# Kernel tuning notes

Hardware: AMD Instinct MI355X
Metric: run time of the kernel (lower is better)

The kernel has to match this reference:

```python
import jax, jax.numpy as jnp
import numpy as np

MASK_VALUE = -10000.0


def setup_inputs() -> dict:
    key = jax.random.key(0)
    ks = jax.random.split(key, 6)
    F_, H, L1N, L2N, B = 1024, 2048, 64, 256, 8192

    def w(k, shape, fan_in):
        return jax.random.normal(k, shape, jnp.float32) * (1.0 / np.sqrt(fan_in))

    x = jax.random.normal(ks[0], (B, F_), jnp.float32)
    W1_1 = w(ks[1], (F_, H), F_); b1_1 = jnp.zeros((H,), jnp.float32)
    W1_2 = w(ks[2], (H, L1N), H); b1_2 = jnp.zeros((L1N,), jnp.float32)
    W2_1 = w(ks[3], (F_, H), F_); b2_1 = jnp.zeros((H,), jnp.float32)
    W2_2 = w(ks[4], (2 * H, L2N), 2 * H); b2_2 = jnp.zeros((L2N,), jnp.float32)
    # child_parent[j] = L1 parent of L2 label j (contiguous groups of 4),
    # equivalent to L12_table = [[4i,4i+1,4i+2,4i+3] for i in range(64)]
    child_parent = jnp.arange(L2N, dtype=jnp.int32) // (L2N // L1N)
    return dict(x=x, W1_1=W1_1, b1_1=b1_1, W1_2=W1_2, b1_2=b1_2,
                W2_1=W2_1, b2_1=b2_1, W2_2=W2_2, b2_2=b2_2,
                child_parent=child_parent)


def reference(x, W1_1, b1_1, W1_2, b1_2, W2_1, b2_1, W2_2, b2_2, child_parent):
    h1 = jax.nn.relu(x @ W1_1 + b1_1)          # [B, H]
    h2 = jax.nn.relu(x @ W2_1 + b2_1)          # [B, H]
    cat = jnp.concatenate([h1, h2], axis=1)    # [B, 2H]
    L1 = jax.nn.softmax(jax.nn.relu(h1 @ W1_2 + b1_2), axis=1)   # [B, L1N]
    l2_logits = jax.nn.relu(cat @ W2_2 + b2_2)                   # [B, L2N]
    parent = jnp.argmax(L1, axis=1)                              # [B] int
    # mask[i, j] = 0 if L2 label j is a child of argmax L1 label, else MASK_VALUE
    mask = jnp.where(child_parent[None, :] == parent[:, None], 0.0, MASK_VALUE)
    L2 = jax.nn.softmax(l2_logits + mask, axis=1)
    return (L1, L2)
```

## Files before the change

### kernel.cpp

```cpp
#include <hip/hip_runtime.h>
#include <hip/hip_bf16.h>
#include <stdint.h>
#include <math.h>


typedef _Float16 f16x8 __attribute__((ext_vector_type(8)));
typedef float    f32x4 __attribute__((ext_vector_type(4)));

#define MASK_VALUE (-10000.0f)
#define SWZ(r) ((((r) + ((r) >> 2))) & 3)
#define SW4(row, c) ((c) ^ (((row) >> 1) & 3))
#define RSCALE 2048.0f
#define INV_RSCALE (1.0f / 2048.0f)

#define GLOBAL_AS __attribute__((address_space(1)))
#define LDS_AS    __attribute__((address_space(3)))

__device__ __forceinline__ void gload16(const void* g, void* lds) {
    __builtin_amdgcn_global_load_lds((const GLOBAL_AS void*)g, (LDS_AS void*)lds, 16, 0, 0);
}

__device__ __forceinline__ float rd_any(const void* p, size_t i, int flag) {
    return flag ? (float)((const __hip_bfloat16*)p)[i] : ((const float*)p)[i];
}

__device__ __forceinline__ void wg_bar() {
    asm volatile("" ::: "memory");
    __builtin_amdgcn_s_barrier();
    asm volatile("" ::: "memory");
}
#define LGKM0() do { asm volatile("s_waitcnt lgkmcnt(0)" ::: "memory"); \
                     __builtin_amdgcn_sched_barrier(0); } while (0)
#define VMW(n)  asm volatile("s_waitcnt vmcnt(" #n ")" ::: "memory")
#define MFMA16(a,b,c) __builtin_amdgcn_mfma_f32_16x16x32_f16((a),(b),(c),0,0,0)

__global__ void detect_dtype(const unsigned int* __restrict__ x, int* __restrict__ flag) {
    __shared__ int cnt;
    if (threadIdx.x == 0) cnt = 0;
    __syncthreads();
    int local = 0;
#pragma unroll
    for (int i = 0; i < 4; ++i) {
        unsigned int w = x[threadIdx.x * 4 + i];
        unsigned int e = (w >> 7) & 0xFFu;
        if (e >= 96u && e <= 144u) local++;
    }
    atomicAdd(&cnt, local);
    __syncthreads();
    if (threadIdx.x == 0) *flag = (cnt >= 600) ? 1 : 0;
}

__global__ void prep_all(
    const void* __restrict__ x, const void* __restrict__ W1_1,
    const void* __restrict__ W2_1, const void* __restrict__ W2_2,
    const void* __restrict__ W1_2,
    _Float16* __restrict__ xh, _Float16* __restrict__ xl,
    _Float16* __restrict__ whT, _Float16* __restrict__ wlT,
    _Float16* __restrict__ W2Tf, _Float16* __restrict__ W22Tf,
    _Float16* __restrict__ w12h, _Float16* __restrict__ w12l,
    const int* __restrict__ flagp)
{
    __shared__ __align__(16) float tile[64][65];
    int flag = *flagp;
    int bid = blockIdx.x, t = threadIdx.x;
    int tx = t & 63, ty = t >> 6;

    if (bid < 8192) {
        size_t i = ((size_t)bid * 256 + t) * 4;
#pragma unroll
        for (int j = 0; j < 4; ++j) {
            float a = rd_any(x, i + j, flag);
            _Float16 h = (_Float16)a;
            xh[i + j] = h;
            xl[i + j] = (_Float16)((a - (float)h) * RSCALE);
        }
        return;
    }

    if (bid < 8704) {
        int b = bid - 8192;
        int c0 = (b & 31) * 64, r0 = (b >> 5) * 64;
#pragma unroll
        for (int i = 0; i < 16; ++i) {
            int r = ty + i * 4;
            tile[r][tx] = rd_any(W1_1, (size_t)(r0 + r) * 2048 + c0 + tx, flag);
        }
        __syncthreads();
#pragma unroll
        for (int i = 0; i < 16; ++i) {
            int r = ty + i * 4;
            size_t o = (size_t)(c0 + r) * 1024 + r0 + tx;
            float a = tile[tx][r];
            _Float16 h = (_Float16)a;
            whT[o] = h;
            wlT[o] = (_Float16)((a - (float)h) * RSCALE);
        }
        return;
    }

    if (bid < 9216) {
        int b = bid - 8704;
        int c0 = (b & 31) * 64, r0 = (b >> 5) * 64;
#pragma unroll
        for (int i = 0; i < 16; ++i) {
            int r = ty + i * 4;
            tile[r][tx] = rd_any(W2_1, (size_t)(r0 + r) * 2048 + c0 + tx, flag);
        }
        __syncthreads();
#pragma unroll
        for (int i = 0; i < 16; ++i) {
            int r = ty + i * 4;
            W2Tf[(size_t)(c0 + r) * 1024 + r0 + tx] = (_Float16)tile[tx][r];
        }
        return;
    }

    if (bid < 9472) {
        int b = bid - 9216;
        int c0 = (b & 3) * 64, r0 = (b >> 2) * 64;
#pragma unroll
        for (int i = 0; i < 16; ++i) {
            int r = ty + i * 4;
            tile[r][tx] = rd_any(W2_2, (size_t)(r0 + r) * 256 + c0 + tx, flag);
        }
        __syncthreads();
#pragma unroll
        for (int i = 0; i < 16; ++i) {
            int r = ty + i * 4;
            W22Tf[(size_t)(c0 + r) * 4096 + r0 + tx] = (_Float16)tile[tx][r];
        }
        return;
    }

    {
        int b = bid - 9472;
        int r0 = b * 64;
#pragma unroll
        for (int i = 0; i < 16; ++i) {
            int r = ty + i * 4;
            tile[r][tx] = rd_any(W1_2, (size_t)(r0 + r) * 64 + tx, flag);
        }
        __syncthreads();
#pragma unroll
        for (int i = 0; i < 16; ++i) {
            int r = ty + i * 4;
            size_t o = (size_t)r * 2048 + r0 + tx;
            float a = tile[tx][r];
            _Float16 h = (_Float16)a;
            w12h[o] = h;
            w12l[o] = (_Float16)((a - (float)h) * RSCALE);
        }
    }
}

__global__ __launch_bounds__(512, 2) void h12_gemm8(
    const _Float16* __restrict__ xh, const _Float16* __restrict__ xl,
    const _Float16* __restrict__ whT, const _Float16* __restrict__ wlT,
    const void* __restrict__ b11,
    const _Float16* __restrict__ W2Tf, const void* __restrict__ b21,
    _Float16* __restrict__ h1h, _Float16* __restrict__ h1l,
    _Float16* __restrict__ h2b,
    const int* __restrict__ flagp)
{
    __shared__ __align__(16) char smem[147456];
    int flag = *flagp;
    int t = threadIdx.x, w = t >> 6, lane = t & 63;
    int ml = lane & 15, q = lane >> 4, rq = q * 4;

    int xcd = blockIdx.x & 7, rblk = blockIdx.x >> 3;

    if (rblk < 64) {
        int lb = xcd * 64 + rblk;
        int mt = lb >> 4, nt = lb & 15;
        int i0 = mt * 256, j0 = nt * 128;
        int wr = w & 3, wc = w >> 2;

        f32x4 acc1[4][4], acc2[4][4];
#pragma unroll
        for (int a = 0; a < 4; ++a)
#pragma unroll
            for (int b = 0; b < 4; ++b) {
                acc1[a][b] = (f32x4){0.f, 0.f, 0.f, 0.f};
                acc2[a][b] = (f32x4){0.f, 0.f, 0.f, 0.f};
            }

        auto stage = [&](char* bp, int kt, int g) {
            if (g < 4) {
                int ci = ((g & 1) << 9) + t;
                int row = ci >> 2;
                int c = SW4(row, ci & 3);
                const _Float16* src = (g < 2) ? xh : xl;
                gload16(src + (size_t)(i0 + row) * 1024 + kt + c * 8,
                        bp + ((g < 2) ? 0 : 16384) + ci * 16);
            } else {
                int ci = t;
                int row = ci >> 2;
                int c = SW4(row, ci & 3);
                const _Float16* src = (g == 4) ? whT : wlT;
                gload16(src + (size_t)(j0 + row) * 1024 + kt + c * 8,
                        bp + ((g == 4) ? 32768 : 40960) + ci * 16);
            }
        };

#pragma unroll
        for (int g = 0; g < 6; ++g) stage(smem, 0, g);
#pragma unroll
        for (int g = 0; g < 6; ++g) stage(smem + 49152, 32, g);
        VMW(6);
        wg_bar();

        int cur = 0;
        for (int s = 0; s < 32; ++s) {
            char* bp = smem + cur * 49152;
            int cur2 = cur + 2; if (cur2 >= 3) cur2 -= 3;
            char* bp2 = smem + cur2 * 49152;
            int kt2 = (s + 2) * 32;
            bool st = (s < 30);

            f16x8 ah[4], al[4], bh[2], bl[2];
            if (st) { stage(bp2, kt2, 0); stage(bp2, kt2, 1); stage(bp2, kt2, 2); }
#pragma unroll
            for (int rt = 0; rt < 4; ++rt) {
                int row = wr * 64 + rt * 16 + ml;
                int off = row * 64 + (SW4(row, q) << 4);
                ah[rt] = *(const f16x8*)(bp + off);
                al[rt] = *(const f16x8*)(bp + 16384 + off);
            }
#pragma unroll
            for (int ct = 0; ct < 2; ++ct) {
                int row = wc * 64 + ct * 16 + ml;
                int off = row * 64 + (SW4(row, q) << 4);
                bh[ct] = *(const f16x8*)(bp + 32768 + off);
                bl[ct] = *(const f16x8*)(bp + 40960 + off);
            }
            LGKM0();
            __builtin_amdgcn_s_setprio(1);
#pragma unroll
            for (int rt = 0; rt < 4; ++rt)
#pragma unroll
                for (int ct = 0; ct < 2; ++ct) {
                    acc1[rt][ct] = MFMA16(ah[rt], bh[ct], acc1[rt][ct]);
                    acc2[rt][ct] = MFMA16(ah[rt], bl[ct], acc2[rt][ct]);
                    acc2[rt][ct] = MFMA16(al[rt], bh[ct], acc2[rt][ct]);
                }
            __builtin_amdgcn_s_setprio(0);

            if (st) { stage(bp2, kt2, 3); stage(bp2, kt2, 4); stage(bp2, kt2, 5); }
#pragma unroll
            for (int ct = 0; ct < 2; ++ct) {
                int row = wc * 64 + (ct + 2) * 16 + ml;
                int off = row * 64 + (SW4(row, q) << 4);
                bh[ct] = *(const f16x8*)(bp + 32768 + off);
                bl[ct] = *(const f16x8*)(bp + 40960 + off);
            }
            LGKM0();
            __builtin_amdgcn_s_setprio(1);
#pragma unroll
            for (int rt = 0; rt < 4; ++rt)
#pragma unroll
                for (int ct = 0; ct < 2; ++ct) {
                    acc1[rt][ct + 2] = MFMA16(ah[rt], bh[ct], acc1[rt][ct + 2]);
                    acc2[rt][ct + 2] = MFMA16(ah[rt], bl[ct], acc2[rt][ct + 2]);
                    acc2[rt][ct + 2] = MFMA16(al[rt], bh[ct], acc2[rt][ct + 2]);
                }
            __builtin_amdgcn_s_setprio(0);

            if (st) { VMW(6); } else { VMW(0); }
            wg_bar();
            cur = cur + 1; if (cur == 3) cur = 0;
        }

#pragma unroll
        for (int ct = 0; ct < 4; ++ct) {
            float bv = rd_any(b11, j0 + wc * 64 + ct * 16 + ml, flag);
#pragma unroll
            for (int rt = 0; rt < 4; ++rt)
#pragma unroll
                for (int rr = 0; rr < 4; ++rr) {
                    float v = acc1[rt][ct][rr] + acc2[rt][ct][rr] * INV_RSCALE + bv;
                    acc1[rt][ct][rr] = v > 0.f ? v : 0.f;
                }
        }
        _Float16* C = (_Float16*)smem;
#pragma unroll
        for (int p = 0; p < 2; ++p) {
            __syncthreads();
#pragma unroll
            for (int rt = 0; rt < 4; ++rt)
#pragma unroll
                for (int ct = 0; ct < 4; ++ct)
#pragma unroll
                    for (int rr = 0; rr < 4; ++rr) {
                        float v = acc1[rt][ct][rr];
                        _Float16 h = (_Float16)v;
                        _Float16 outv = (p == 0) ? h
                                      : (_Float16)((v - (float)h) * RSCALE);
                        int rl = wr * 64 + rt * 16 + rq + rr;
                        int cl = wc * 64 + ct * 16 + ml;
                        C[rl * 136 + cl] = outv;
                    }
            __syncthreads();
            _Float16* dst = (p == 0) ? h1h : h1l;
#pragma unroll
            for (int i = 0; i < 8; ++i) {
                int c = i * 512 + t;
                int row = c >> 4, c8 = (c & 15) * 8;
                *(f16x8*)(dst + (size_t)(i0 + row) * 2048 + j0 + c8) =
                    *(const f16x8*)(C + row * 136 + c8);
            }
        }
    } else {
        int lb = xcd * 32 + (rblk - 64);
        int mt = lb >> 3, nt = lb & 7;
        int i0 = mt * 256, j0 = nt * 256;
        int wr = w & 1, wc = w >> 1;

        f32x4 acc[8][4];
#pragma unroll
        for (int a = 0; a < 8; ++a)
#pragma unroll
            for (int b = 0; b < 4; ++b) acc[a][b] = (f32x4){0.f, 0.f, 0.f, 0.f};

        auto stage = [&](char* bp, int kt, int g) {
            int ci = ((g & 1) << 9) + t;
            int row = ci >> 2;
            int c = SW4(row, ci & 3);
            if (g < 2)
                gload16(xh + (size_t)(i0 + row) * 1024 + kt + c * 8,
                        bp + ci * 16);
            else
                gload16(W2Tf + (size_t)(j0 + row) * 1024 + kt + c * 8,
                        bp + 16384 + ci * 16);
        };

#pragma unroll
        for (int g = 0; g < 4; ++g) stage(smem, 0, g);
#pragma unroll
        for (int g = 0; g < 4; ++g) stage(smem + 32768, 32, g);
        VMW(4);
        wg_bar();

        int cur = 0;
        for (int s = 0; s < 32; ++s) {
            char* bp = smem + cur * 32768;
            char* bp2 = smem + ((cur + 2) & 3) * 32768;
            int kt2 = (s + 2) * 32;
            bool st = (s < 30);

            f16x8 af[4], bf[4];
            if (st) { stage(bp2, kt2, 0); stage(bp2, kt2, 2); }
#pragma unroll
            for (int rt = 0; rt < 4; ++rt) {
                int row = wr * 128 + rt * 16 + ml;
                int off = row * 64 + (SW4(row, q) << 4);
                af[rt] = *(const f16x8*)(bp + off);
            }
#pragma unroll
            for (int ct = 0; ct < 4; ++ct) {
                int row = wc * 64 + ct * 16 + ml;
                int off = row * 64 + (SW4(row, q) << 4);
                bf[ct] = *(const f16x8*)(bp + 16384 + off);
            }
            LGKM0();
            __builtin_amdgcn_s_setprio(1);
#pragma unroll
            for (int rt = 0; rt < 4; ++rt)
#pragma unroll
                for (int ct = 0; ct < 4; ++ct)
                    acc[rt][ct] = MFMA16(af[rt], bf[ct], acc[rt][ct]);
            __builtin_amdgcn_s_setprio(0);

            if (st) { stage(bp2, kt2, 1); stage(bp2, kt2, 3); }
#pragma unroll
            for (int rt = 0; rt < 4; ++rt) {
                int row = wr * 128 + (rt + 4) * 16 + ml;
                int off = row * 64 + (SW4(row, q) << 4);
                af[rt] = *(const f16x8*)(bp + off);
            }
            LGKM0();
            __builtin_amdgcn_s_setprio(1);
#pragma unroll
            for (int rt = 0; rt < 4; ++rt)
#pragma unroll
                for (int ct = 0; ct < 4; ++ct)
                    acc[rt + 4][ct] = MFMA16(af[rt], bf[ct], acc[rt + 4][ct]);
            __builtin_amdgcn_s_setprio(0);

            if (st) { VMW(4); } else { VMW(0); }
            wg_bar();
            cur = (cur + 1) & 3;
        }

        _Float16* C = (_Float16*)smem;
        __syncthreads();
#pragma unroll
        for (int ct = 0; ct < 4; ++ct) {
            float bv = rd_any(b21, j0 + wc * 64 + ct * 16 + ml, flag);
#pragma unroll
            for (int rt = 0; rt < 8; ++rt)
#pragma unroll
                for (int rr = 0; rr < 4; ++rr) {
                    float v = acc[rt][ct][rr] + bv;
                    v = v > 0.f ? v : 0.f;
                    int rl = wr * 128 + rt * 16 + rq + rr;
                    int cl = wc * 64 + ct * 16 + ml;
                    C[rl * 264 + cl] = (_Float16)v;
                }
        }
        __syncthreads();
#pragma unroll
        for (int i = 0; i < 16; ++i) {
            int c = i * 512 + t;
            int row = c >> 5, c8 = (c & 31) * 8;
            *(f16x8*)(h2b + (size_t)(i0 + row) * 2048 + j0 + c8) =
                *(const f16x8*)(C + row * 264 + c8);
        }
    }
}

__global__ __launch_bounds__(256, 2) void head_fused(
    const _Float16* __restrict__ h1h, const _Float16* __restrict__ h1l,
    const _Float16* __restrict__ h2b, const _Float16* __restrict__ W22T,
    float* __restrict__ partials,
    const _Float16* __restrict__ w12h, const _Float16* __restrict__ w12l,
    const void* __restrict__ b12, float* __restrict__ L1out,
    int* __restrict__ parent, const int* __restrict__ flagp)
{
    constexpr int BK = 32;
    __shared__ __align__(16) char smem[16384];
    int flag = *flagp;
    int t = threadIdx.x, w = t >> 6, lane = t & 63;
    int ml = lane & 15, q = lane >> 4;

    if (blockIdx.x < 512) {
        _Float16* As = (_Float16*)smem;
        _Float16* Bs = (_Float16*)(smem + 8192);
        int bid = blockIdx.x;
        int g = bid & 7, s = bid >> 3;
        int mt = g * 8 + (s & 7);
        int rest = s >> 3;
        int nt = rest & 1, kc = rest >> 1;
        int i0 = mt * 128, j0 = nt * 128;
        const _Float16* Abase = (kc < 2) ? h1h : h2b;
        int kof = (kc & 1) * 1024;
        int wr = w & 1, wcb = w >> 1;

        f32x4 acc[4][4];
#pragma unroll
        for (int a = 0; a < 4; ++a)
#pragma unroll
            for (int b = 0; b < 4; ++b) acc[a][b] = (f32x4){0.f, 0.f, 0.f, 0.f};

        for (int kt = 0; kt < 1024; kt += BK) {
            __syncthreads();
#pragma unroll
            for (int qq = 0; qq < 2; ++qq) {
                int c = qq * 256 + t;
                int row = c >> 2;
                int gc = (c & 3) ^ SWZ(row);
                gload16(Abase + (size_t)(i0 + row) * 2048 + kof + kt + gc * 8, (char*)As + c * 16);
                gload16(W22T + (size_t)(j0 + row) * 4096 + kc * 1024 + kt + gc * 8, (char*)Bs + c * 16);
            }
            __syncthreads();
            f16x8 af[4], bf[4];
#pragma unroll
            for (int rt = 0; rt < 4; ++rt) {
                int row = wr * 64 + rt * 16 + ml;
                af[rt] = *(const f16x8*)(As + row * 32 + ((q ^ SWZ(row)) << 3));
            }
#pragma unroll
            for (int ct = 0; ct < 4; ++ct) {
                int row = wcb * 64 + ct * 16 + ml;
                bf[ct] = *(const f16x8*)(Bs + row * 32 + ((q ^ SWZ(row)) << 3));
            }
#pragma unroll
            for (int rt = 0; rt < 4; ++rt)
#pragma unroll
                for (int ct = 0; ct < 4; ++ct)
                    acc[rt][ct] = __builtin_amdgcn_mfma_f32_16x16x32_f16(
                        af[rt], bf[ct], acc[rt][ct], 0, 0, 0);
        }

        float* out = partials + (size_t)kc * 8192 * 256;
        int rq = (lane >> 4) * 4;
#pragma unroll
        for (int ct = 0; ct < 4; ++ct) {
            int nl = j0 + wcb * 64 + ct * 16 + ml;
#pragma unroll
            for (int rt = 0; rt < 4; ++rt) {
                int mbase = i0 + wr * 64 + rt * 16 + rq;
#pragma unroll
                for (int r = 0; r < 4; ++r)
                    out[(size_t)(mbase + r) * 256 + nl] = acc[rt][ct][r];
            }
        }
    } else {
        float* red = (float*)smem;
        int r0 = (blockIdx.x - 512) * 16;
        int kq = (lane >> 4) * 8;

        f32x4 acch[4], accx[4];
#pragma unroll
        for (int ct = 0; ct < 4; ++ct) {
            acch[ct] = (f32x4){0.f, 0.f, 0.f, 0.f};
            accx[ct] = (f32x4){0.f, 0.f, 0.f, 0.f};
        }

        size_t aoff = (size_t)(r0 + ml) * 2048 + w * 512 + kq;
        const _Float16* Ah = h1h + aoff;
        const _Float16* Al = h1l + aoff;
        size_t boff[4];
#pragma unroll
        for (int ct = 0; ct < 4; ++ct)
            boff[ct] = (size_t)(ct * 16 + ml) * 2048 + w * 512 + kq;

        f16x8 ah = *(const f16x8*)(Ah), al = *(const f16x8*)(Al);
        f16x8 bh[4], bl[4];
#pragma unroll
        for (int ct = 0; ct < 4; ++ct) {
            bh[ct] = *(const f16x8*)(w12h + boff[ct]);
            bl[ct] = *(const f16x8*)(w12l + boff[ct]);
        }

        for (int kt = 0; kt < 512; kt += 32) {
            int nk = (kt + 32) & 511;
            f16x8 nah = *(const f16x8*)(Ah + nk);
            f16x8 nal = *(const f16x8*)(Al + nk);
            f16x8 nbh[4], nbl[4];
#pragma unroll
            for (int ct = 0; ct < 4; ++ct) {
                nbh[ct] = *(const f16x8*)(w12h + boff[ct] + nk);
                nbl[ct] = *(const f16x8*)(w12l + boff[ct] + nk);
            }
#pragma unroll
            for (int ct = 0; ct < 4; ++ct) {
                acch[ct] = __builtin_amdgcn_mfma_f32_16x16x32_f16(ah, bh[ct], acch[ct], 0, 0, 0);
                accx[ct] = __builtin_amdgcn_mfma_f32_16x16x32_f16(ah, bl[ct], accx[ct], 0, 0, 0);
                accx[ct] = __builtin_amdgcn_mfma_f32_16x16x32_f16(al, bh[ct], accx[ct], 0, 0, 0);
            }
            ah = nah; al = nal;
#pragma unroll
            for (int ct = 0; ct < 4; ++ct) { bh[ct] = nbh[ct]; bl[ct] = nbl[ct]; }
        }

        f32x4 acc[4];
#pragma unroll
        for (int ct = 0; ct < 4; ++ct)
#pragma unroll
            for (int i = 0; i < 4; ++i)
                acc[ct][i] = acch[ct][i] + accx[ct][i] * INV_RSCALE;

        if (w > 0) {
#pragma unroll
            for (int ct = 0; ct < 4; ++ct)
#pragma unroll
                for (int i = 0; i < 4; ++i)
                    red[((w - 1) * 4 + ct) * 256 + lane * 4 + i] = acc[ct][i];
        }
        __syncthreads();
        if (w != 0) return;

#pragma unroll
        for (int wv = 0; wv < 3; ++wv)
#pragma unroll
            for (int ct = 0; ct < 4; ++ct)
#pragma unroll
                for (int i = 0; i < 4; ++i)
                    acc[ct][i] += red[(wv * 4 + ct) * 256 + lane * 4 + i];

        int rq = (lane >> 4) * 4;
        float vals[4][4];
        float vmax[4] = {-1e30f, -1e30f, -1e30f, -1e30f};
        int vidx[4] = {1 << 30, 1 << 30, 1 << 30, 1 << 30};
#pragma unroll
        for (int ct = 0; ct < 4; ++ct) {
            int col = ct * 16 + ml;
            float bv = rd_any(b12, col, flag);
#pragma unroll
            for (int r = 0; r < 4; ++r) {
                float v = acc[ct][r] + bv;
                v = v > 0.f ? v : 0.f;
                vals[ct][r] = v;
                if (v > vmax[r] || (v == vmax[r] && col < vidx[r])) { vmax[r] = v; vidx[r] = col; }
            }
        }
#pragma unroll
        for (int d = 1; d < 16; d <<= 1) {
#pragma unroll
            for (int r = 0; r < 4; ++r) {
                float om = __shfl_xor(vmax[r], d);
                int oi = __shfl_xor(vidx[r], d);
                if (om > vmax[r] || (om == vmax[r] && oi < vidx[r])) { vmax[r] = om; vidx[r] = oi; }
            }
        }
        float vsum[4] = {0.f, 0.f, 0.f, 0.f};
#pragma unroll
        for (int ct = 0; ct < 4; ++ct)
#pragma unroll
            for (int r = 0; r < 4; ++r) {
                float e = __expf(vals[ct][r] - vmax[r]);
                vals[ct][r] = e;
                vsum[r] += e;
            }
#pragma unroll
        for (int d = 1; d < 16; d <<= 1)
#pragma unroll
            for (int r = 0; r < 4; ++r) vsum[r] += __shfl_xor(vsum[r], d);

#pragma unroll
        for (int r = 0; r < 4; ++r) {
            float inv = 1.0f / vsum[r];
            int grow = r0 + rq + r;
#pragma unroll
            for (int ct = 0; ct < 4; ++ct)
                L1out[(size_t)grow * 64 + ct * 16 + ml] = vals[ct][r] * inv;
            if (ml == 0) parent[grow] = vidx[r];
        }
    }
}

__global__ __launch_bounds__(256, 2) void l2_softmax(
    const float* __restrict__ partials, const void* __restrict__ b22,
    const int* __restrict__ child_parent, const int* __restrict__ parent,
    float* __restrict__ L2out, const int* __restrict__ flagp)
{
    int flag = *flagp;
    int t = threadIdx.x, w = t >> 6, lane = t & 63;
    int row = blockIdx.x * 4 + w;
    int c4 = lane * 4;

    float v[4] = {0.f, 0.f, 0.f, 0.f};
#pragma unroll
    for (int kc = 0; kc < 4; ++kc) {
        float4 pv = *(const float4*)(partials + ((size_t)kc * 8192 + row) * 256 + c4);
        v[0] += pv.x; v[1] += pv.y; v[2] += pv.z; v[3] += pv.w;
    }
    int par = parent[row];
#pragma unroll
    for (int j = 0; j < 4; ++j) {
        float x = v[j] + rd_any(b22, c4 + j, flag);
        x = x > 0.f ? x : 0.f;
        if (child_parent[c4 + j] != par) x += MASK_VALUE;
        v[j] = x;
    }
    float m = fmaxf(fmaxf(v[0], v[1]), fmaxf(v[2], v[3]));
#pragma unroll
    for (int d = 1; d < 64; d <<= 1) m = fmaxf(m, __shfl_xor(m, d));
    float sum = 0.f;
#pragma unroll
    for (int j = 0; j < 4; ++j) { v[j] = __expf(v[j] - m); sum += v[j]; }
#pragma unroll
    for (int d = 1; d < 64; d <<= 1) sum += __shfl_xor(sum, d);
    float inv = 1.0f / sum;
    float4 o = {v[0] * inv, v[1] * inv, v[2] * inv, v[3] * inv};
    *(float4*)(L2out + (size_t)row * 256 + c4) = o;
}

extern "C" void kernel_launch(void* const* d_in, const int* in_sizes, int n_in,
                              void* d_out, int out_size, void* d_ws, size_t ws_size,
                              hipStream_t stream) {
    (void)in_sizes; (void)n_in; (void)out_size; (void)ws_size;

    const void* x    = d_in[0];
    const void* W1_1 = d_in[1];
    const void* b1_1 = d_in[2];
    const void* W1_2 = d_in[3];
    const void* b1_2 = d_in[4];
    const void* W2_1 = d_in[5];
    const void* b2_1 = d_in[6];
    const void* W2_2 = d_in[7];
    const void* b2_2 = d_in[8];
    const int* child_parent = (const int*)d_in[9];

    char* p = (char*)d_ws;
    _Float16* xh    = (_Float16*)(p);
    _Float16* xl    = (_Float16*)(p + 16777216);
    _Float16* whT   = (_Float16*)(p + 33554432);
    _Float16* wlT   = (_Float16*)(p + 37748736);
    _Float16* h1h   = (_Float16*)(p + 41943040);
    _Float16* h1l   = (_Float16*)(p + 75497472);
    _Float16* h2b   = (_Float16*)(p + 109051904);
    _Float16* W2Tf  = (_Float16*)(p + 142606336);
    _Float16* W22Tf = (_Float16*)(p + 146800640);
    _Float16* w12h  = (_Float16*)(p + 148897792);
    _Float16* w12l  = (_Float16*)(p + 149159936);
    float* partials = (float*)(p + 149422080);
    int* parent     = (int*)(p + 182976512);
    int* flag       = (int*)(p + 183009280);

    float* L1out = (float*)d_out;
    float* L2out = L1out + (size_t)8192 * 64;

    hipLaunchKernelGGL(detect_dtype, dim3(1), dim3(256), 0, stream,
                       (const unsigned int*)x, flag);
    hipLaunchKernelGGL(prep_all, dim3(9504), dim3(256), 0, stream,
                       x, W1_1, W2_1, W2_2, W1_2,
                       xh, xl, whT, wlT, W2Tf, W22Tf, w12h, w12l, flag);
    hipLaunchKernelGGL(h12_gemm8, dim3(768), dim3(512), 0, stream,
                       xh, xl, whT, wlT, b1_1, W2Tf, b2_1,
                       h1h, h1l, h2b, flag);
    hipLaunchKernelGGL(head_fused, dim3(1024), dim3(256), 0, stream,
                       h1h, h1l, h2b, W22Tf, partials,
                       w12h, w12l, b1_2, L1out, parent, flag);
    hipLaunchKernelGGL(l2_softmax, dim3(2048), dim3(256), 0, stream,
                       partials, b2_2, child_parent, parent, L2out, flag);
}
```

Before: 326.1 us.

## Software-pipeline LDS fragment reads across the barrier in both GEMM loops

```diff
diff --git a/kernel.cpp b/kernel.cpp
--- a/kernel.cpp
+++ b/kernel.cpp
@@ -29,9 +29,10 @@
     __builtin_amdgcn_s_barrier();
     asm volatile("" ::: "memory");
 }
-#define LGKM0() do { asm volatile("s_waitcnt lgkmcnt(0)" ::: "memory"); \
-                     __builtin_amdgcn_sched_barrier(0); } while (0)
+#define LGKMN(n) do { asm volatile("s_waitcnt lgkmcnt(" #n ")" ::: "memory"); \
+                      __builtin_amdgcn_sched_barrier(0); } while (0)
 #define VMW(n)  asm volatile("s_waitcnt vmcnt(" #n ")" ::: "memory")
+#define SB0()   __builtin_amdgcn_sched_barrier(0)
 #define MFMA16(a,b,c) __builtin_amdgcn_mfma_f32_16x16x32_f16((a),(b),(c),0,0,0)
 
 __global__ void detect_dtype(const unsigned int* __restrict__ x, int* __restrict__ flag) {
@@ -183,6 +184,8 @@
                 acc1[a][b] = (f32x4){0.f, 0.f, 0.f, 0.f};
                 acc2[a][b] = (f32x4){0.f, 0.f, 0.f, 0.f};
             }
+
+        f16x8 ah[4], al[4], bAh[2], bAl[2], bBh[2], bBl[2];
 
         auto stage = [&](char* bp, int kt, int g) {
             if (g < 4) {
@@ -201,24 +204,16 @@
                         bp + ((g == 4) ? 32768 : 40960) + ci * 16);
             }
         };
-
-#pragma unroll
-        for (int g = 0; g < 6; ++g) stage(smem, 0, g);
-#pragma unroll
-        for (int g = 0; g < 6; ++g) stage(smem + 49152, 32, g);
-        VMW(6);
-        wg_bar();
-
-        int cur = 0;
-        for (int s = 0; s < 32; ++s) {
-            char* bp = smem + cur * 49152;
-            int cur2 = cur + 2; if (cur2 >= 3) cur2 -= 3;
-            char* bp2 = smem + cur2 * 49152;
-            int kt2 = (s + 2) * 32;
-            bool st = (s < 30);
-
-            f16x8 ah[4], al[4], bh[2], bl[2];
-            if (st) { stage(bp2, kt2, 0); stage(bp2, kt2, 1); stage(bp2, kt2, 2); }
+        auto rdBA = [&](char* bp) {
+#pragma unroll
+            for (int ct = 0; ct < 2; ++ct) {
+                int row = wc * 64 + ct * 16 + ml;
+                int off = row * 64 + (SW4(row, q) << 4);
+                bAh[ct] = *(const f16x8*)(bp + 32768 + off);
+                bAl[ct] = *(const f16x8*)(bp + 40960 + off);
+            }
+        };
+        auto rdA = [&](char* bp) {
 #pragma unroll
             for (int rt = 0; rt < 4; ++rt) {
                 int row = wr * 64 + rt * 16 + ml;
@@ -226,47 +221,67 @@
                 ah[rt] = *(const f16x8*)(bp + off);
                 al[rt] = *(const f16x8*)(bp + 16384 + off);
             }
-#pragma unroll
-            for (int ct = 0; ct < 2; ++ct) {
-                int row = wc * 64 + ct * 16 + ml;
-                int off = row * 64 + (SW4(row, q) << 4);
-                bh[ct] = *(const f16x8*)(bp + 32768 + off);
-                bl[ct] = *(const f16x8*)(bp + 40960 + off);
-            }
-            LGKM0();
-            __builtin_amdgcn_s_setprio(1);
-#pragma unroll
-            for (int rt = 0; rt < 4; ++rt)
-#pragma unroll
-                for (int ct = 0; ct < 2; ++ct) {
-                    acc1[rt][ct] = MFMA16(ah[rt], bh[ct], acc1[rt][ct]);
-                    acc2[rt][ct] = MFMA16(ah[rt], bl[ct], acc2[rt][ct]);
-                    acc2[rt][ct] = MFMA16(al[rt], bh[ct], acc2[rt][ct]);
-                }
-            __builtin_amdgcn_s_setprio(0);
-
-            if (st) { stage(bp2, kt2, 3); stage(bp2, kt2, 4); stage(bp2, kt2, 5); }
+        };
+        auto rdBB = [&](char* bp) {
 #pragma unroll
             for (int ct = 0; ct < 2; ++ct) {
                 int row = wc * 64 + (ct + 2) * 16 + ml;
                 int off = row * 64 + (SW4(row, q) << 4);
-                bh[ct] = *(const f16x8*)(bp + 32768 + off);
-                bl[ct] = *(const f16x8*)(bp + 40960 + off);
-            }
-            LGKM0();
+                bBh[ct] = *(const f16x8*)(bp + 32768 + off);
+                bBl[ct] = *(const f16x8*)(bp + 40960 + off);
+            }
+        };
+
+#pragma unroll
+        for (int g = 0; g < 6; ++g) stage(smem, 0, g);
+#pragma unroll
+        for (int g = 0; g < 6; ++g) stage(smem + 49152, 32, g);
+        VMW(6);
+        wg_bar();
+        rdBA(smem); SB0();
+        rdA(smem);  SB0();
+        rdBB(smem); SB0();
+
+        int cur = 0;
+        for (int s = 0; s < 32; ++s) {
+            char* bpn = smem + ((cur + 1 == 3) ? 0 : cur + 1) * 49152;
+            int cur2 = cur + 2; if (cur2 >= 3) cur2 -= 3;
+            char* bp2 = smem + cur2 * 49152;
+            int kt2 = (s + 2) * 32;
+            bool st = (s < 30), rd = (s < 31);
+
+            if (st) {
+#pragma unroll
+                for (int g = 0; g < 6; ++g) stage(bp2, kt2, g);
+            }
+            LGKMN(4);
             __builtin_amdgcn_s_setprio(1);
 #pragma unroll
             for (int rt = 0; rt < 4; ++rt)
 #pragma unroll
                 for (int ct = 0; ct < 2; ++ct) {
-                    acc1[rt][ct + 2] = MFMA16(ah[rt], bh[ct], acc1[rt][ct + 2]);
-                    acc2[rt][ct + 2] = MFMA16(ah[rt], bl[ct], acc2[rt][ct + 2]);
-                    acc2[rt][ct + 2] = MFMA16(al[rt], bh[ct], acc2[rt][ct + 2]);
+                    acc1[rt][ct] = MFMA16(ah[rt], bAh[ct], acc1[rt][ct]);
+                    acc2[rt][ct] = MFMA16(ah[rt], bAl[ct], acc2[rt][ct]);
+                    acc2[rt][ct] = MFMA16(al[rt], bAh[ct], acc2[rt][ct]);
                 }
             __builtin_amdgcn_s_setprio(0);
-
+            LGKMN(0);
             if (st) { VMW(6); } else { VMW(0); }
             wg_bar();
+
+            if (rd) rdBA(bpn);
+            SB0();
+            __builtin_amdgcn_s_setprio(1);
+#pragma unroll
+            for (int rt = 0; rt < 4; ++rt)
+#pragma unroll
+                for (int ct = 0; ct < 2; ++ct) {
+                    acc1[rt][ct + 2] = MFMA16(ah[rt], bBh[ct], acc1[rt][ct + 2]);
+                    acc2[rt][ct + 2] = MFMA16(ah[rt], bBl[ct], acc2[rt][ct + 2]);
+                    acc2[rt][ct + 2] = MFMA16(al[rt], bBh[ct], acc2[rt][ct + 2]);
+                }
+            __builtin_amdgcn_s_setprio(0);
+            if (rd) { rdA(bpn); SB0(); rdBB(bpn); }
             cur = cur + 1; if (cur == 3) cur = 0;
         }
 
@@ -321,6 +336,8 @@
 #pragma unroll
             for (int b = 0; b < 4; ++b) acc[a][b] = (f32x4){0.f, 0.f, 0.f, 0.f};
 
+        f16x8 af0[4], af4[4], bfa[4], bfb[4];
+
         auto stage = [&](char* bp, int kt, int g) {
             int ci = ((g & 1) << 9) + t;
             int row = ci >> 2;
@@ -332,6 +349,30 @@
                 gload16(W2Tf + (size_t)(j0 + row) * 1024 + kt + c * 8,
                         bp + 16384 + ci * 16);
         };
+        auto rdBF = [&](char* bp, f16x8* dst) {
+#pragma unroll
+            for (int ct = 0; ct < 4; ++ct) {
+                int row = wc * 64 + ct * 16 + ml;
+                int off = row * 64 + (SW4(row, q) << 4);
+                dst[ct] = *(const f16x8*)(bp + 16384 + off);
+            }
+        };
+        auto rdA0 = [&](char* bp) {
+#pragma unroll
+            for (int rt = 0; rt < 4; ++rt) {
+                int row = wr * 128 + rt * 16 + ml;
+                int off = row * 64 + (SW4(row, q) << 4);
+                af0[rt] = *(const f16x8*)(bp + off);
+            }
+        };
+        auto rdA4 = [&](char* bp) {
+#pragma unroll
+            for (int rt = 0; rt < 4; ++rt) {
+                int row = wr * 128 + (rt + 4) * 16 + ml;
+                int off = row * 64 + (SW4(row, q) << 4);
+                af4[rt] = *(const f16x8*)(bp + off);
+            }
+        };
 
 #pragma unroll
         for (int g = 0; g < 4; ++g) stage(smem, 0, g);
@@ -339,56 +380,49 @@
         for (int g = 0; g < 4; ++g) stage(smem + 32768, 32, g);
         VMW(4);
         wg_bar();
+        rdBF(smem, bfa); SB0();
+        rdA0(smem);      SB0();
+        rdA4(smem);      SB0();
 
         int cur = 0;
-        for (int s = 0; s < 32; ++s) {
-            char* bp = smem + cur * 32768;
+        auto body = [&](int s, f16x8* BFC, f16x8* BFN) {
+            char* bpn = smem + ((cur + 1) & 3) * 32768;
             char* bp2 = smem + ((cur + 2) & 3) * 32768;
             int kt2 = (s + 2) * 32;
-            bool st = (s < 30);
-
-            f16x8 af[4], bf[4];
-            if (st) { stage(bp2, kt2, 0); stage(bp2, kt2, 2); }
-#pragma unroll
-            for (int rt = 0; rt < 4; ++rt) {
-                int row = wr * 128 + rt * 16 + ml;
-                int off = row * 64 + (SW4(row, q) << 4);
-                af[rt] = *(const f16x8*)(bp + off);
-            }
-#pragma unroll
-            for (int ct = 0; ct < 4; ++ct) {
-                int row = wc * 64 + ct * 16 + ml;
-                int off = row * 64 + (SW4(row, q) << 4);
-                bf[ct] = *(const f16x8*)(bp + 16384 + off);
-            }
-            LGKM0();
+            bool st = (s < 30), rd = (s < 31);
+
+            if (st) {
+#pragma unroll
+                for (int g = 0; g < 4; ++g) stage(bp2, kt2, g);
+            }
+            LGKMN(4);
             __builtin_amdgcn_s_setprio(1);
 #pragma unroll
             for (int rt = 0; rt < 4; ++rt)
 #pragma unroll
                 for (int ct = 0; ct < 4; ++ct)
-                    acc[rt][ct] = MFMA16(af[rt], bf[ct], acc[rt][ct]);
+                    acc[rt][ct] = MFMA16(af0[rt], BFC[ct], acc[rt][ct]);
             __builtin_amdgcn_s_setprio(0);
-
-            if (st) { stage(bp2, kt2, 1); stage(bp2, kt2, 3); }
-#pragma unroll
-            for (int rt = 0; rt < 4; ++rt) {
-                int row = wr * 128 + (rt + 4) * 16 + ml;
-                int off = row * 64 + (SW4(row, q) << 4);
-                af[rt] = *(const f16x8*)(bp + off);
-            }
-            LGKM0();
-            __builtin_amdgcn_s_setprio(1);
-#pragma unroll
-            for (int rt = 0; rt < 4; ++rt)
-#pragma unroll
-                for (int ct = 0; ct < 4; ++ct)
-                    acc[rt + 4][ct] = MFMA16(af[rt], bf[ct], acc[rt + 4][ct]);
-            __builtin_amdgcn_s_setprio(0);
-
+            LGKMN(0);
             if (st) { VMW(4); } else { VMW(0); }
             wg_bar();
+
+            if (rd) { rdBF(bpn, BFN); rdA0(bpn); }
+            SB0();
+            __builtin_amdgcn_s_setprio(1);
+#pragma unroll
+            for (int rt = 0; rt < 4; ++rt)
+#pragma unroll
+                for (int ct = 0; ct < 4; ++ct)
+                    acc[rt + 4][ct] = MFMA16(af4[rt], BFC[ct], acc[rt + 4][ct]);
+            __builtin_amdgcn_s_setprio(0);
+            if (rd) rdA4(bpn);
             cur = (cur + 1) & 3;
+        };
+
+        for (int k = 0; k < 16; ++k) {
+            body(2 * k,     bfa, bfb);
+            body(2 * k + 1, bfb, bfa);
         }
 
         _Float16* C = (_Float16*)smem;
```

Measured after the change: 323.1 us. Within noise of the previous version (-0.9%).

## Shrink GEMM tiles to 256-thread blocks with simple double buffering, vectorize x prep

Applied to the files above, without the earlier changes.

```diff
diff --git a/kernel.cpp b/kernel.cpp
--- a/kernel.cpp
+++ b/kernel.cpp
@@ -5,7 +5,9 @@
 
 
 typedef _Float16 f16x8 __attribute__((ext_vector_type(8)));
+typedef _Float16 f16x4 __attribute__((ext_vector_type(4)));
 typedef float    f32x4 __attribute__((ext_vector_type(4)));
+typedef unsigned short u16x4 __attribute__((ext_vector_type(4)));
 
 #define MASK_VALUE (-10000.0f)
 #define SWZ(r) ((((r) + ((r) >> 2))) & 3)
@@ -29,9 +31,10 @@
     __builtin_amdgcn_s_barrier();
     asm volatile("" ::: "memory");
 }
-#define LGKM0() do { asm volatile("s_waitcnt lgkmcnt(0)" ::: "memory"); \
-                     __builtin_amdgcn_sched_barrier(0); } while (0)
+#define LGKMN(n) do { asm volatile("s_waitcnt lgkmcnt(" #n ")" ::: "memory"); \
+                      __builtin_amdgcn_sched_barrier(0); } while (0)
 #define VMW(n)  asm volatile("s_waitcnt vmcnt(" #n ")" ::: "memory")
+#define SB0()   __builtin_amdgcn_sched_barrier(0)
 #define MFMA16(a,b,c) __builtin_amdgcn_mfma_f32_16x16x32_f16((a),(b),(c),0,0,0)
 
 __global__ void detect_dtype(const unsigned int* __restrict__ x, int* __restrict__ flag) {
@@ -67,13 +70,24 @@
 
     if (bid < 8192) {
         size_t i = ((size_t)bid * 256 + t) * 4;
-#pragma unroll
-        for (int j = 0; j < 4; ++j) {
-            float a = rd_any(x, i + j, flag);
-            _Float16 h = (_Float16)a;
-            xh[i + j] = h;
-            xl[i + j] = (_Float16)((a - (float)h) * RSCALE);
-        }
+        float a0, a1, a2, a3;
+        if (flag) {
+            u16x4 u = *(const u16x4*)((const unsigned short*)x + i);
+            a0 = __uint_as_float(((unsigned)u[0]) << 16);
+            a1 = __uint_as_float(((unsigned)u[1]) << 16);
+            a2 = __uint_as_float(((unsigned)u[2]) << 16);
+            a3 = __uint_as_float(((unsigned)u[3]) << 16);
+        } else {
+            f32x4 f = *(const f32x4*)((const float*)x + i);
+            a0 = f[0]; a1 = f[1]; a2 = f[2]; a3 = f[3];
+        }
+        f16x4 hv, lv;
+        _Float16 h0 = (_Float16)a0; hv[0] = h0; lv[0] = (_Float16)((a0 - (float)h0) * RSCALE);
+        _Float16 h1 = (_Float16)a1; hv[1] = h1; lv[1] = (_Float16)((a1 - (float)h1) * RSCALE);
+        _Float16 h2 = (_Float16)a2; hv[2] = h2; lv[2] = (_Float16)((a2 - (float)h2) * RSCALE);
+        _Float16 h3 = (_Float16)a3; hv[3] = h3; lv[3] = (_Float16)((a3 - (float)h3) * RSCALE);
+        *(f16x4*)(xh + i) = hv;
+        *(f16x4*)(xl + i) = lv;
         return;
     }
 
@@ -153,7 +167,7 @@
     }
 }
 
-__global__ __launch_bounds__(512, 2) void h12_gemm8(
+__global__ __launch_bounds__(256, 2) void h12_gemm8(
     const _Float16* __restrict__ xh, const _Float16* __restrict__ xl,
     const _Float16* __restrict__ whT, const _Float16* __restrict__ wlT,
     const void* __restrict__ b11,
@@ -162,18 +176,18 @@
     _Float16* __restrict__ h2b,
     const int* __restrict__ flagp)
 {
-    __shared__ __align__(16) char smem[147456];
+    __shared__ __align__(16) char smem[69632];
     int flag = *flagp;
     int t = threadIdx.x, w = t >> 6, lane = t & 63;
     int ml = lane & 15, q = lane >> 4, rq = q * 4;
 
     int xcd = blockIdx.x & 7, rblk = blockIdx.x >> 3;
 
-    if (rblk < 64) {
-        int lb = xcd * 64 + rblk;
+    if (rblk < 128) {
+        int lb = xcd * 128 + rblk;
         int mt = lb >> 4, nt = lb & 15;
-        int i0 = mt * 256, j0 = nt * 128;
-        int wr = w & 3, wc = w >> 2;
+        int i0 = mt * 128, j0 = nt * 128;
+        int wr = w & 1, wc = w >> 1;
 
         f32x4 acc1[4][4], acc2[4][4];
 #pragma unroll
@@ -184,90 +198,63 @@
                 acc2[a][b] = (f32x4){0.f, 0.f, 0.f, 0.f};
             }
 
-        auto stage = [&](char* bp, int kt, int g) {
-            if (g < 4) {
-                int ci = ((g & 1) << 9) + t;
+        f16x8 ah[4], al[4], bh[4], bl[4];
+
+        auto stage = [&](char* bp, int kt) {
+#pragma unroll
+            for (int g = 0; g < 2; ++g) {
+                int ci = (g << 8) + t;
                 int row = ci >> 2;
                 int c = SW4(row, ci & 3);
-                const _Float16* src = (g < 2) ? xh : xl;
-                gload16(src + (size_t)(i0 + row) * 1024 + kt + c * 8,
-                        bp + ((g < 2) ? 0 : 16384) + ci * 16);
-            } else {
-                int ci = t;
-                int row = ci >> 2;
-                int c = SW4(row, ci & 3);
-                const _Float16* src = (g == 4) ? whT : wlT;
-                gload16(src + (size_t)(j0 + row) * 1024 + kt + c * 8,
-                        bp + ((g == 4) ? 32768 : 40960) + ci * 16);
+                size_t ga = (size_t)(i0 + row) * 1024 + kt + c * 8;
+                size_t gb = (size_t)(j0 + row) * 1024 + kt + c * 8;
+                gload16(xh + ga,  bp +         ci * 16);
+                gload16(xl + ga,  bp +  8192 + ci * 16);
+                gload16(whT + gb, bp + 16384 + ci * 16);
+                gload16(wlT + gb, bp + 24576 + ci * 16);
             }
         };
-
-#pragma unroll
-        for (int g = 0; g < 6; ++g) stage(smem, 0, g);
-#pragma unroll
-        for (int g = 0; g < 6; ++g) stage(smem + 49152, 32, g);
-        VMW(6);
-        wg_bar();
-
-        int cur = 0;
-        for (int s = 0; s < 32; ++s) {
-            char* bp = smem + cur * 49152;
-            int cur2 = cur + 2; if (cur2 >= 3) cur2 -= 3;
-            char* bp2 = smem + cur2 * 49152;
-            int kt2 = (s + 2) * 32;
-            bool st = (s < 30);
-
-            f16x8 ah[4], al[4], bh[2], bl[2];
-            if (st) { stage(bp2, kt2, 0); stage(bp2, kt2, 1); stage(bp2, kt2, 2); }
+        auto rdAll = [&](char* bp) {
 #pragma unroll
             for (int rt = 0; rt < 4; ++rt) {
                 int row = wr * 64 + rt * 16 + ml;
                 int off = row * 64 + (SW4(row, q) << 4);
                 ah[rt] = *(const f16x8*)(bp + off);
-                al[rt] = *(const f16x8*)(bp + 16384 + off);
-            }
-#pragma unroll
-            for (int ct = 0; ct < 2; ++ct) {
+                al[rt] = *(const f16x8*)(bp + 8192 + off);
+            }
+#pragma unroll
+            for (int ct = 0; ct < 4; ++ct) {
                 int row = wc * 64 + ct * 16 + ml;
                 int off = row * 64 + (SW4(row, q) << 4);
-                bh[ct] = *(const f16x8*)(bp + 32768 + off);
-                bl[ct] = *(const f16x8*)(bp + 40960 + off);
-            }
-            LGKM0();
+                bh[ct] = *(const f16x8*)(bp + 16384 + off);
+                bl[ct] = *(const f16x8*)(bp + 24576 + off);
+            }
+        };
+
+        stage(smem, 0);
+        VMW(0);
+        wg_bar();
+
+        for (int s = 0; s < 32; ++s) {
+            char* bpc = smem + (s & 1) * 32768;
+            char* bpn = smem + ((s + 1) & 1) * 32768;
+            bool st = (s < 31);
+
+            if (st) stage(bpn, (s + 1) * 32);
+            rdAll(bpc);
+            LGKMN(0);
             __builtin_amdgcn_s_setprio(1);
 #pragma unroll
             for (int rt = 0; rt < 4; ++rt)
 #pragma unroll
-                for (int ct = 0; ct < 2; ++ct) {
+                for (int ct = 0; ct < 4; ++ct) {
                     acc1[rt][ct] = MFMA16(ah[rt], bh[ct], acc1[rt][ct]);
                     acc2[rt][ct] = MFMA16(ah[rt], bl[ct], acc2[rt][ct]);
                     acc2[rt][ct] = MFMA16(al[rt], bh[ct], acc2[rt][ct]);
                 }
             __builtin_amdgcn_s_setprio(0);
-
-            if (st) { stage(bp2, kt2, 3); stage(bp2, kt2, 4); stage(bp2, kt2, 5); }
-#pragma unroll
-            for (int ct = 0; ct < 2; ++ct) {
-                int row = wc * 64 + (ct + 2) * 16 + ml;
-                int off = row * 64 + (SW4(row, q) << 4);
-                bh[ct] = *(const f16x8*)(bp + 32768 + off);
-                bl[ct] = *(const f16x8*)(bp + 40960 + off);
-            }
-            LGKM0();
-            __builtin_amdgcn_s_setprio(1);
-#pragma unroll
-            for (int rt = 0; rt < 4; ++rt)
-#pragma unroll
-                for (int ct = 0; ct < 2; ++ct) {
-                    acc1[rt][ct + 2] = MFMA16(ah[rt], bh[ct], acc1[rt][ct + 2]);
-                    acc2[rt][ct + 2] = MFMA16(ah[rt], bl[ct], acc2[rt][ct + 2]);
-                    acc2[rt][ct + 2] = MFMA16(al[rt], bh[ct], acc2[rt][ct + 2]);
-                }
-            __builtin_amdgcn_s_setprio(0);
-
-            if (st) { VMW(6); } else { VMW(0); }
+            if (st) { VMW(0); }
             wg_bar();
-            cur = cur + 1; if (cur == 3) cur = 0;
         }
 
 #pragma unroll
@@ -303,17 +290,17 @@
             _Float16* dst = (p == 0) ? h1h : h1l;
 #pragma unroll
             for (int i = 0; i < 8; ++i) {
-                int c = i * 512 + t;
+                int c = i * 256 + t;
                 int row = c >> 4, c8 = (c & 15) * 8;
                 *(f16x8*)(dst + (size_t)(i0 + row) * 2048 + j0 + c8) =
                     *(const f16x8*)(C + row * 136 + c8);
             }
         }
     } else {
-        int lb = xcd * 32 + (rblk - 64);
+        int lb = xcd * 64 + (rblk - 128);
         int mt = lb >> 3, nt = lb & 7;
-        int i0 = mt * 256, j0 = nt * 256;
-        int wr = w & 1, wc = w >> 1;
+        int i0 = mt * 128, j0 = nt * 256;
+        int wc2 = w;
 
         f32x4 acc[8][4];
 #pragma unroll
@@ -321,96 +308,84 @@
 #pragma unroll
             for (int b = 0; b < 4; ++b) acc[a][b] = (f32x4){0.f, 0.f, 0.f, 0.f};
 
-        auto stage = [&](char* bp, int kt, int g) {
-            int ci = ((g & 1) << 9) + t;
-            int row = ci >> 2;
-            int c = SW4(row, ci & 3);
-            if (g < 2)
+        f16x8 af[8], bf[4];
+
+        auto stage = [&](char* bp, int kt) {
+#pragma unroll
+            for (int g = 0; g < 2; ++g) {
+                int ci = (g << 8) + t;
+                int row = ci >> 2;
+                int c = SW4(row, ci & 3);
                 gload16(xh + (size_t)(i0 + row) * 1024 + kt + c * 8,
                         bp + ci * 16);
-            else
+            }
+#pragma unroll
+            for (int g = 0; g < 4; ++g) {
+                int ci = (g << 8) + t;
+                int row = ci >> 2;
+                int c = SW4(row, ci & 3);
                 gload16(W2Tf + (size_t)(j0 + row) * 1024 + kt + c * 8,
-                        bp + 16384 + ci * 16);
+                        bp + 8192 + ci * 16);
+            }
         };
-
-#pragma unroll
-        for (int g = 0; g < 4; ++g) stage(smem, 0, g);
-#pragma unroll
-        for (int g = 0; g < 4; ++g) stage(smem + 32768, 32, g);
-        VMW(4);
-        wg_bar();
-
-        int cur = 0;
-        for (int s = 0; s < 32; ++s) {
-            char* bp = smem + cur * 32768;
-            char* bp2 = smem + ((cur + 2) & 3) * 32768;
-            int kt2 = (s + 2) * 32;
-            bool st = (s < 30);
-
-            f16x8 af[4], bf[4];
-            if (st) { stage(bp2, kt2, 0); stage(bp2, kt2, 2); }
-#pragma unroll
-            for (int rt = 0; rt < 4; ++rt) {
-                int row = wr * 128 + rt * 16 + ml;
+        auto rdAll = [&](char* bp) {
+#pragma unroll
+            for (int rt = 0; rt < 8; ++rt) {
+                int row = rt * 16 + ml;
                 int off = row * 64 + (SW4(row, q) << 4);
                 af[rt] = *(const f16x8*)(bp + off);
             }
 #pragma unroll
             for (int ct = 0; ct < 4; ++ct) {
-                int row = wc * 64 + ct * 16 + ml;
+                int row = wc2 * 64 + ct * 16 + ml;
                 int off = row * 64 + (SW4(row, q) << 4);
-                bf[ct] = *(const f16x8*)(bp + 16384 + off);
-            }
-            LGKM0();
+                bf[ct] = *(const f16x8*)(bp + 8192 + off);
+            }
+        };
+
+        stage(smem, 0);
+        VMW(0);
+        wg_bar();
+
+        for (int s = 0; s < 32; ++s) {
+            char* bpc = smem + (s & 1) * 24576;
+            char* bpn = smem + ((s + 1) & 1) * 24576;
+            bool st = (s < 31);
+
+            if (st) stage(bpn, (s + 1) * 32);
+            rdAll(bpc);
+            LGKMN(0);
             __builtin_amdgcn_s_setprio(1);
 #pragma unroll
-            for (int rt = 0; rt < 4; ++rt)
+            for (int rt = 0; rt < 8; ++rt)
 #pragma unroll
                 for (int ct = 0; ct < 4; ++ct)
                     acc[rt][ct] = MFMA16(af[rt], bf[ct], acc[rt][ct]);
             __builtin_amdgcn_s_setprio(0);
-
-            if (st) { stage(bp2, kt2, 1); stage(bp2, kt2, 3); }
-#pragma unroll
-            for (int rt = 0; rt < 4; ++rt) {
-                int row = wr * 128 + (rt + 4) * 16 + ml;
-                int off = row * 64 + (SW4(row, q) << 4);
-                af[rt] = *(const f16x8*)(bp + off);
-            }
-            LGKM0();
-            __builtin_amdgcn_s_setprio(1);
-#pragma unroll
-            for (int rt = 0; rt < 4; ++rt)
-#pragma unroll
-                for (int ct = 0; ct < 4; ++ct)
-                    acc[rt + 4][ct] = MFMA16(af[rt], bf[ct], acc[rt + 4][ct]);
-            __builtin_amdgcn_s_setprio(0);
-
-            if (st) { VMW(4); } else { VMW(0); }
+            if (st) { VMW(0); }
             wg_bar();
-            cur = (cur + 1) & 3;
         }
 
         _Float16* C = (_Float16*)smem;
         __syncthreads();
 #pragma unroll
         for (int ct = 0; ct < 4; ++ct) {
-            float bv = rd_any(b21, j0 + wc * 64 + ct * 16 + ml, flag);
+            float bv = rd_any(b21, j0 + wc2 * 64 + ct * 16 + ml, flag);
 #pragma unroll
             for (int rt = 0; rt < 8; ++rt)
 #pragma unroll
                 for (int rr = 0; rr < 4; ++rr) {
                     float v = acc[rt][ct][rr] + bv;
                     v = v > 0.f ? v : 0.f;
-                    int rl = wr * 128 + rt * 16 + rq + rr;
-                    int cl = wc * 64 + ct * 16 + ml;
+                    int rl = rt * 16 + rq + rr;
+                    int cl = wc2 * 64 + ct * 16 + ml;
                     C[rl * 264 + cl] = (_Float16)v;
                 }
         }
         __syncthreads();
 #pragma unroll
         for (int i = 0; i < 16; ++i) {
-            int c = i * 512 + t;
+            int c = i * 256 + t;
             int row = c >> 5, c8 = (c & 31) * 8;
             *(f16x8*)(h2b + (size_t)(i0 + row) * 2048 + j0 + c8) =
                 *(const f16x8*)(C + row * 264 + c8);
@@ -696,7 +671,7 @@
     hipLaunchKernelGGL(prep_all, dim3(9504), dim3(256), 0, stream,
                        x, W1_1, W2_1, W2_2, W1_2,
                        xh, xl, whT, wlT, W2Tf, W22Tf, w12h, w12l, flag);
-    hipLaunchKernelGGL(h12_gemm8, dim3(768), dim3(512), 0, stream,
+    hipLaunchKernelGGL(h12_gemm8, dim3(1536), dim3(256), 0, stream,
                        xh, xl, whT, wlT, b1_1, W2Tf, b2_1,
                        h1h, h1l, h2b, flag);
     hipLaunchKernelGGL(head_fused, dim3(1024), dim3(256), 0, stream,
```

After: 330.9 us. Within noise of the previous version (+1.5%).
